# Kernel optimization log

Hardware: AMD Instinct MI355X
Metric: run time of the kernel (lower is better)

Reference implementation:

```python
import jax, jax.numpy as jnp
import numpy as np

N_PER_DEG = 30000
MAX_DEG = 6
MIN_DEG = 0
N_ATOMS = N_PER_DEG * (MAX_DEG + 1)  # 210000, atoms sorted by degree
N_FEAT = 128
NB_FILTER = 128
NB_AFFINE = 2 * MAX_DEG + (1 - MIN_DEG)  # 13


def setup_inputs() -> dict:
    key = jax.random.key(0)
    ks = jax.random.split(key, 2 + MAX_DEG)
    atoms = jax.random.normal(ks[0], (N_ATOMS, N_FEAT), dtype=jnp.float32)
    # glorot-ish scale for the 13 affine weights
    W = jax.random.normal(ks[1], (NB_AFFINE, N_FEAT, NB_FILTER), dtype=jnp.float32) * (1.0 / np.sqrt(N_FEAT))
    b = jnp.zeros((NB_AFFINE, NB_FILTER), dtype=jnp.float32)
    # deg_slice[d] = (start, count) for degree d in 0..MAX_DEG; equal-size buckets
    deg_slice = jnp.asarray(
        np.stack([np.arange(MAX_DEG + 1) * N_PER_DEG,
                  np.full(MAX_DEG + 1, N_PER_DEG)], axis=1).astype(np.int32))
    inp = {"atoms": atoms, "W": W, "b": b, "deg_slice": deg_slice}
    for d in range(1, MAX_DEG + 1):
        inp[f"adj{d}"] = jax.random.randint(ks[1 + d], (N_PER_DEG, d), 0, N_ATOMS, dtype=jnp.int32)
    return inp


def reference(atoms, W, b, deg_slice, adj1, adj2, adj3, adj4, adj5, adj6):
    """Degree-bucketed graph convolution (deepchem GraphConv, linear activation).

    W ordering matches the original iterator: for deg=1..MAX_DEG the pair
    (rel=W[2*(deg-1)], self=W[2*(deg-1)+1]), then deg-0 self uses W[2*MAX_DEG].
    Output concat order: deg 0 bucket first, then deg 1..MAX_DEG.
    """
    adjs = [adj1, adj2, adj3, adj4, adj5, adj6]
    ds = np.asarray(deg_slice)  # structural constant: static slice bounds
    outs = [None] * (MAX_DEG + 1 - MIN_DEG)
    # deg 0: self-affine only
    s0, c0 = int(ds[0, 0]), int(ds[0, 1])
    outs[0] = atoms[s0:s0 + c0] @ W[2 * MAX_DEG] + b[2 * MAX_DEG]
    for deg in range(1, MAX_DEG + 1):
        s, c = int(ds[deg, 0]), int(ds[deg, 1])
        # gather neighbors of each degree-deg atom and sum: (c, deg, F) -> (c, F)
        rel = jnp.take(atoms, adjs[deg - 1], axis=0).sum(axis=1)
        out = (rel @ W[2 * (deg - 1)] + b[2 * (deg - 1)]
               + atoms[s:s + c] @ W[2 * (deg - 1) + 1] + b[2 * (deg - 1) + 1])
        outs[deg] = out
    return jnp.concatenate(outs, axis=0)  # (N_ATOMS, NB_FILTER)
```

## Files before the change

### kernel.cpp

```cpp
#include <hip/hip_runtime.h>
#include <hip/hip_bf16.h>

#define NPD 30000
#define NF  128
#define MAXDEG 6
#define LDK2 264

typedef __attribute__((ext_vector_type(8))) short short8;
typedef __attribute__((ext_vector_type(4))) float floatx4;

__device__ __forceinline__ unsigned short f2bf(float f) {
    __hip_bfloat16 h = __float2bfloat16(f);
    return __builtin_bit_cast(unsigned short, h);
}
__device__ __forceinline__ uint4 pack16B(float4 a, float4 b) {
    uint4 v;
    v.x = (unsigned)f2bf(a.x) | ((unsigned)f2bf(a.y) << 16);
    v.y = (unsigned)f2bf(a.z) | ((unsigned)f2bf(a.w) << 16);
    v.z = (unsigned)f2bf(b.x) | ((unsigned)f2bf(b.y) << 16);
    v.w = (unsigned)f2bf(b.z) | ((unsigned)f2bf(b.w) << 16);
    return v;
}

__global__ __launch_bounds__(256) void wt_kernel(const float* __restrict__ W,
                                                 unsigned short* __restrict__ Wt) {
    __shared__ unsigned short t[32][33];
    const int bx = blockIdx.x;
    const int a  = bx >> 4;
    const int k0 = ((bx >> 2) & 3) * 32, n0 = (bx & 3) * 32;
    const int tx = threadIdx.x & 31, ty = threadIdx.x >> 5;
    const float*    Wp  = W  + (size_t)a * NF * NF;
    unsigned short* Wtp = Wt + (size_t)a * NF * NF;
#pragma unroll
    for (int i = 0; i < 32; i += 8)
        t[ty + i][tx] = f2bf(Wp[(size_t)(k0 + ty + i) * NF + (n0 + tx)]);
    __syncthreads();
#pragma unroll
    for (int i = 0; i < 32; i += 8)
        Wtp[(size_t)(n0 + ty + i) * NF + (k0 + tx)] = t[tx][ty + i];
}

template <int DEG>
__device__ __forceinline__ void fused_work(
    const float* __restrict__ atoms, const unsigned short* __restrict__ Wt,
    const float* __restrict__ bvec, const int* __restrict__ adj,
    float* __restrict__ out, unsigned short* __restrict__ sA)
{
    const int tid  = threadIdx.x;
    const int lane = tid & 63, wave = tid >> 6;
    const int nb = lane & 15;
    const int kq = (lane >> 4) * 8;
    const int col0 = wave * 32;
    const int row0 = blockIdx.x * 32;
    const int valid = min(32, NPD - row0);
    const int row0g = DEG * NPD + row0;
    const int wi_self = (DEG == 0) ? 12 : (2 * DEG - 1);
    const int wi_rel  = (DEG > 0) ? 2 * (DEG - 1) : 0;

    const int r0 = tid >> 4,          ch0 = (tid & 15) * 8;
    const int r1 = (tid >> 4) + 16,   ch1 = ch0;
    const int rr0 = min(r0, valid - 1), rr1 = min(r1, valid - 1);
    const float4* sp0 = (const float4*)(atoms + (size_t)(row0g + rr0) * NF + ch0);
    const float4* sp1 = (const float4*)(atoms + (size_t)(row0g + rr1) * NF + ch1);
    float4 sv0 = sp0[0], sv1 = sp0[1], sv2 = sp1[0], sv3 = sp1[1];

    if constexpr (DEG > 0) {
        const int gr  = tid >> 3;
        const int gc  = (tid & 7) * 16;
        const int grr = min(gr, valid - 1);
        const int* arow = adj + (size_t)(row0 + grr) * DEG;
        int idxs[DEG];
#pragma unroll
        for (int j = 0; j < DEG; ++j) idxs[j] = arow[j];

        *(uint4*)&sA[r0 * LDK2 + ch0] = pack16B(sv0, sv1);
        *(uint4*)&sA[r1 * LDK2 + ch1] = pack16B(sv2, sv3);

        float s[16];
#pragma unroll
        for (int i = 0; i < 16; ++i) s[i] = 0.f;
        float4 q0, q1, q2, q3, n0, n1, n2, n3;
        {
            const float4* p = (const float4*)(atoms + (size_t)idxs[0] * NF + gc);
            q0 = p[0]; q1 = p[1]; q2 = p[2]; q3 = p[3];
        }
#pragma unroll
        for (int j = 0; j < DEG; ++j) {
            if (j + 1 < DEG) {
                const float4* p = (const float4*)(atoms + (size_t)idxs[j + 1] * NF + gc);
                n0 = p[0]; n1 = p[1]; n2 = p[2]; n3 = p[3];
            }
            s[0]  += q0.x; s[1]  += q0.y; s[2]  += q0.z; s[3]  += q0.w;
            s[4]  += q1.x; s[5]  += q1.y; s[6]  += q1.z; s[7]  += q1.w;
            s[8]  += q2.x; s[9]  += q2.y; s[10] += q2.z; s[11] += q2.w;
            s[12] += q3.x; s[13] += q3.y; s[14] += q3.z; s[15] += q3.w;
            q0 = n0; q1 = n1; q2 = n2; q3 = n3;
        }
        uint4 w0 = pack16B(make_float4(s[0], s[1], s[2], s[3]),
                           make_float4(s[4], s[5], s[6], s[7]));
        uint4 w1 = pack16B(make_float4(s[8], s[9], s[10], s[11]),
                           make_float4(s[12], s[13], s[14], s[15]));
        *(uint4*)&sA[gr * LDK2 + NF + gc]     = w0;
        *(uint4*)&sA[gr * LDK2 + NF + gc + 8] = w1;
    } else {
        *(uint4*)&sA[r0 * LDK2 + ch0] = pack16B(sv0, sv1);
        *(uint4*)&sA[r1 * LDK2 + ch1] = pack16B(sv2, sv3);
    }
    __syncthreads();

    floatx4 acc[2][2];
#pragma unroll
    for (int i = 0; i < 2; i++)
#pragma unroll
        for (int j = 0; j < 2; j++) acc[i][j] = (floatx4){0.f, 0.f, 0.f, 0.f};

    constexpr int NKK = (DEG > 0) ? 8 : 4;
#pragma unroll
    for (int kk = 0; kk < NKK; ++kk) {
        const int wi = (kk < 4) ? wi_self : wi_rel;
        const unsigned short* Wp = Wt + (size_t)wi * NF * NF;
        short8 bfr[2];
#pragma unroll
        for (int nt = 0; nt < 2; ++nt)
            bfr[nt] = *(const short8*)(Wp + (size_t)(col0 + nt * 16 + nb) * NF
                                          + (kk & 3) * 32 + kq);
        short8 af[2];
#pragma unroll
        for (int mt = 0; mt < 2; ++mt)
            af[mt] = *(const short8*)&sA[(mt * 16 + nb) * LDK2 + kk * 32 + kq];
#pragma unroll
        for (int mt = 0; mt < 2; ++mt)
#pragma unroll
            for (int nt = 0; nt < 2; ++nt)
                acc[mt][nt] = __builtin_amdgcn_mfma_f32_16x16x32_bf16(
                    af[mt], bfr[nt], acc[mt][nt], 0, 0, 0);
    }

    float bias[2];
#pragma unroll
    for (int nt = 0; nt < 2; ++nt) {
        const int n = col0 + nt * 16 + nb;
        float bv = bvec[wi_self * NF + n];
        if (DEG > 0) bv += bvec[wi_rel * NF + n];
        bias[nt] = bv;
    }
    const int rq = (lane >> 4) * 4;
#pragma unroll
    for (int mt = 0; mt < 2; ++mt) {
#pragma unroll
        for (int reg = 0; reg < 4; ++reg) {
            const int r = mt * 16 + rq + reg;
            if (r < valid) {
                float* op = out + (size_t)(row0g + r) * NF;
#pragma unroll
                for (int nt = 0; nt < 2; ++nt)
                    __builtin_nontemporal_store(acc[mt][nt][reg] + bias[nt],
                                                op + col0 + nt * 16 + nb);
            }
        }
    }
}

__global__ __launch_bounds__(256) void fused_kernel(
    const float* __restrict__ atoms, const unsigned short* __restrict__ Wt,
    const float* __restrict__ bvec,
    const int* __restrict__ adj1, const int* __restrict__ adj2,
    const int* __restrict__ adj3, const int* __restrict__ adj4,
    const int* __restrict__ adj5, const int* __restrict__ adj6,
    float* __restrict__ out)
{
    __shared__ unsigned short sA[32 * LDK2];
    switch (blockIdx.y) {
        case 0: fused_work<0>(atoms, Wt, bvec, nullptr, out, sA); break;
        case 1: fused_work<1>(atoms, Wt, bvec, adj1,    out, sA); break;
        case 2: fused_work<2>(atoms, Wt, bvec, adj2,    out, sA); break;
        case 3: fused_work<3>(atoms, Wt, bvec, adj3,    out, sA); break;
        case 4: fused_work<4>(atoms, Wt, bvec, adj4,    out, sA); break;
        case 5: fused_work<5>(atoms, Wt, bvec, adj5,    out, sA); break;
        default: fused_work<6>(atoms, Wt, bvec, adj6,   out, sA); break;
    }
}

__global__ __launch_bounds__(128) void naive_kernel(
    const float* __restrict__ atoms, const float* __restrict__ W,
    const float* __restrict__ b,
    const int* __restrict__ adj1, const int* __restrict__ adj2,
    const int* __restrict__ adj3, const int* __restrict__ adj4,
    const int* __restrict__ adj5, const int* __restrict__ adj6,
    float* __restrict__ out)
{
    const int i = blockIdx.x;
    const int deg = i / NPD, r = i - deg * NPD, n = threadIdx.x;
    __shared__ float selfr[NF], relr[NF];
    selfr[n] = atoms[(size_t)i * NF + n];
    float rv = 0.f;
    if (deg > 0) {
        const int* adjs[6] = {adj1, adj2, adj3, adj4, adj5, adj6};
        const int* adj = adjs[deg - 1];
        for (int j = 0; j < deg; ++j)
            rv += atoms[(size_t)adj[(size_t)r * deg + j] * NF + n];
    }
    relr[n] = rv;
    __syncthreads();
    const int ws  = (deg == 0) ? 12 : 2 * deg - 1;
    const int wrl = 2 * (deg - 1);
    float acc = b[ws * NF + n] + ((deg > 0) ? b[wrl * NF + n] : 0.f);
    for (int k = 0; k < NF; ++k) {
        acc += selfr[k] * W[(size_t)ws * NF * NF + (size_t)k * NF + n];
        if (deg > 0) acc += relr[k] * W[(size_t)wrl * NF * NF + (size_t)k * NF + n];
    }
    out[(size_t)i * NF + n] = acc;
}

extern "C" void kernel_launch(void* const* d_in, const int* in_sizes, int n_in,
                              void* d_out, int out_size, void* d_ws, size_t ws_size,
                              hipStream_t stream) {
    const float* atoms = (const float*)d_in[0];
    const float* W     = (const float*)d_in[1];
    const float* b     = (const float*)d_in[2];
    const int* adj1 = (const int*)d_in[4];
    const int* adj2 = (const int*)d_in[5];
    const int* adj3 = (const int*)d_in[6];
    const int* adj4 = (const int*)d_in[7];
    const int* adj5 = (const int*)d_in[8];
    const int* adj6 = (const int*)d_in[9];

    const size_t wt_bytes = (size_t)13 * NF * NF * sizeof(unsigned short);

    if (ws_size >= wt_bytes) {
        unsigned short* Wt = (unsigned short*)d_ws;
        wt_kernel<<<208, 256, 0, stream>>>(W, Wt);
        const int gx = (NPD + 31) / 32;
        fused_kernel<<<dim3(gx, 7), 256, 0, stream>>>(
            atoms, Wt, b, adj1, adj2, adj3, adj4, adj5, adj6, (float*)d_out);
    } else {
        naive_kernel<<<NPD * (MAXDEG + 1), NF, 0, stream>>>(
            atoms, W, b, adj1, adj2, adj3, adj4, adj5, adj6, (float*)d_out);
    }
}
```

Baseline: 269.6 us.

## Pre-convert atoms to bf16 in a prep pass and gather bf16 rows

Adds a prep kernel that converts the whole atoms matrix to bf16 in workspace, merged with the weight transpose into one launch. The fused kernel then loads self rows and gathered neighbour rows as bf16, halving gather bytes, and issues all neighbour loads up front before accumulating. The cost is an extra full read of fp32 atoms plus a bf16 write. Neighbour sums now use bf16-rounded inputs, which adds rounding error before accumulation.

```diff
diff --git a/kernel.cpp b/kernel.cpp
--- a/kernel.cpp
+++ b/kernel.cpp
@@ -6,12 +6,18 @@
 #define MAXDEG 6
 #define LDK2 264
 
+#define CVT_BLOCKS 13125
+#define WT_BLOCKS  208
+
 typedef __attribute__((ext_vector_type(8))) short short8;
 typedef __attribute__((ext_vector_type(4))) float floatx4;
 
 __device__ __forceinline__ unsigned short f2bf(float f) {
     __hip_bfloat16 h = __float2bfloat16(f);
     return __builtin_bit_cast(unsigned short, h);
+}
+__device__ __forceinline__ float bf2f(unsigned short u) {
+    unsigned v = ((unsigned)u) << 16; return __builtin_bit_cast(float, v);
 }
 __device__ __forceinline__ uint4 pack16B(float4 a, float4 b) {
     uint4 v;
@@ -21,30 +27,55 @@
     v.w = (unsigned)f2bf(b.z) | ((unsigned)f2bf(b.w) << 16);
     return v;
 }
-
-__global__ __launch_bounds__(256) void wt_kernel(const float* __restrict__ W,
-                                                 unsigned short* __restrict__ Wt) {
+__device__ __forceinline__ uint4 pack16Bv(floatx4 a, floatx4 b) {
+    uint4 v;
+    v.x = (unsigned)f2bf(a.x) | ((unsigned)f2bf(a.y) << 16);
+    v.y = (unsigned)f2bf(a.z) | ((unsigned)f2bf(a.w) << 16);
+    v.z = (unsigned)f2bf(b.x) | ((unsigned)f2bf(b.y) << 16);
+    v.w = (unsigned)f2bf(b.z) | ((unsigned)f2bf(b.w) << 16);
+    return v;
+}
+__device__ __forceinline__ void addu4(float* s, uint4 h) {
+    s[0] += bf2f((unsigned short)h.x); s[1] += bf2f((unsigned short)(h.x >> 16));
+    s[2] += bf2f((unsigned short)h.y); s[3] += bf2f((unsigned short)(h.y >> 16));
+    s[4] += bf2f((unsigned short)h.z); s[5] += bf2f((unsigned short)(h.z >> 16));
+    s[6] += bf2f((unsigned short)h.w); s[7] += bf2f((unsigned short)(h.w >> 16));
+}
+
+__global__ __launch_bounds__(256) void prep_kernel(
+    const float* __restrict__ atoms, const float* __restrict__ W,
+    unsigned short* __restrict__ atomsH, unsigned short* __restrict__ Wt)
+{
     __shared__ unsigned short t[32][33];
     const int bx = blockIdx.x;
-    const int a  = bx >> 4;
-    const int k0 = ((bx >> 2) & 3) * 32, n0 = (bx & 3) * 32;
-    const int tx = threadIdx.x & 31, ty = threadIdx.x >> 5;
-    const float*    Wp  = W  + (size_t)a * NF * NF;
-    unsigned short* Wtp = Wt + (size_t)a * NF * NF;
-#pragma unroll
-    for (int i = 0; i < 32; i += 8)
-        t[ty + i][tx] = f2bf(Wp[(size_t)(k0 + ty + i) * NF + (n0 + tx)]);
-    __syncthreads();
-#pragma unroll
-    for (int i = 0; i < 32; i += 8)
-        Wtp[(size_t)(n0 + ty + i) * NF + (k0 + tx)] = t[tx][ty + i];
-}
-
-template <int DEG>
+    if (bx < WT_BLOCKS) {
+        const int a  = bx >> 4;
+        const int k0 = ((bx >> 2) & 3) * 32, n0 = (bx & 3) * 32;
+        const int tx = threadIdx.x & 31, ty = threadIdx.x >> 5;
+        const float*    Wp  = W  + (size_t)a * NF * NF;
+        unsigned short* Wtp = Wt + (size_t)a * NF * NF;
+#pragma unroll
+        for (int i = 0; i < 32; i += 8)
+            t[ty + i][tx] = f2bf(Wp[(size_t)(k0 + ty + i) * NF + (n0 + tx)]);
+        __syncthreads();
+#pragma unroll
+        for (int i = 0; i < 32; i += 8)
+            Wtp[(size_t)(n0 + ty + i) * NF + (k0 + tx)] = t[tx][ty + i];
+    } else {
+        const size_t i = (size_t)(bx - WT_BLOCKS) * 256 + threadIdx.x;
+        const floatx4* p = (const floatx4*)(atoms + i * 8);
+        floatx4 a = __builtin_nontemporal_load(p);
+        floatx4 b = __builtin_nontemporal_load(p + 1);
+        ((uint4*)atomsH)[i] = pack16Bv(a, b);
+    }
+}
+
+template <int DEG, bool BF16A>
 __device__ __forceinline__ void fused_work(
-    const float* __restrict__ atoms, const unsigned short* __restrict__ Wt,
-    const float* __restrict__ bvec, const int* __restrict__ adj,
-    float* __restrict__ out, unsigned short* __restrict__ sA)
+    const float* __restrict__ atomsF, const unsigned short* __restrict__ atomsH,
+    const unsigned short* __restrict__ Wt, const float* __restrict__ bvec,
+    const int* __restrict__ adj, float* __restrict__ out,
+    unsigned short* __restrict__ sA)
 {
     const int tid  = threadIdx.x;
     const int lane = tid & 63, wave = tid >> 6;
@@ -57,12 +88,21 @@
     const int wi_self = (DEG == 0) ? 12 : (2 * DEG - 1);
     const int wi_rel  = (DEG > 0) ? 2 * (DEG - 1) : 0;
 
-    const int r0 = tid >> 4,          ch0 = (tid & 15) * 8;
-    const int r1 = (tid >> 4) + 16,   ch1 = ch0;
+    const int r0 = tid >> 4,        ch0 = (tid & 15) * 8;
+    const int r1 = r0 + 16;
     const int rr0 = min(r0, valid - 1), rr1 = min(r1, valid - 1);
-    const float4* sp0 = (const float4*)(atoms + (size_t)(row0g + rr0) * NF + ch0);
-    const float4* sp1 = (const float4*)(atoms + (size_t)(row0g + rr1) * NF + ch1);
-    float4 sv0 = sp0[0], sv1 = sp0[1], sv2 = sp1[0], sv3 = sp1[1];
+    if (BF16A) {
+        uint4 s0 = *(const uint4*)(atomsH + (size_t)(row0g + rr0) * NF + ch0);
+        uint4 s1 = *(const uint4*)(atomsH + (size_t)(row0g + rr1) * NF + ch0);
+        *(uint4*)&sA[r0 * LDK2 + ch0] = s0;
+        *(uint4*)&sA[r1 * LDK2 + ch0] = s1;
+    } else {
+        const float4* sp0 = (const float4*)(atomsF + (size_t)(row0g + rr0) * NF + ch0);
+        const float4* sp1 = (const float4*)(atomsF + (size_t)(row0g + rr1) * NF + ch0);
+        float4 a0 = sp0[0], a1 = sp0[1], a2 = sp1[0], a3 = sp1[1];
+        *(uint4*)&sA[r0 * LDK2 + ch0] = pack16B(a0, a1);
+        *(uint4*)&sA[r1 * LDK2 + ch0] = pack16B(a2, a3);
+    }
 
     if constexpr (DEG > 0) {
         const int gr  = tid >> 3;
@@ -73,28 +113,41 @@
 #pragma unroll
         for (int j = 0; j < DEG; ++j) idxs[j] = arow[j];
 
-        *(uint4*)&sA[r0 * LDK2 + ch0] = pack16B(sv0, sv1);
-        *(uint4*)&sA[r1 * LDK2 + ch1] = pack16B(sv2, sv3);
-
         float s[16];
 #pragma unroll
         for (int i = 0; i < 16; ++i) s[i] = 0.f;
-        float4 q0, q1, q2, q3, n0, n1, n2, n3;
-        {
-            const float4* p = (const float4*)(atoms + (size_t)idxs[0] * NF + gc);
-            q0 = p[0]; q1 = p[1]; q2 = p[2]; q3 = p[3];
-        }
-#pragma unroll
-        for (int j = 0; j < DEG; ++j) {
-            if (j + 1 < DEG) {
-                const float4* p = (const float4*)(atoms + (size_t)idxs[j + 1] * NF + gc);
-                n0 = p[0]; n1 = p[1]; n2 = p[2]; n3 = p[3];
-            }
-            s[0]  += q0.x; s[1]  += q0.y; s[2]  += q0.z; s[3]  += q0.w;
-            s[4]  += q1.x; s[5]  += q1.y; s[6]  += q1.z; s[7]  += q1.w;
-            s[8]  += q2.x; s[9]  += q2.y; s[10] += q2.z; s[11] += q2.w;
-            s[12] += q3.x; s[13] += q3.y; s[14] += q3.z; s[15] += q3.w;
-            q0 = n0; q1 = n1; q2 = n2; q3 = n3;
+
+        if (BF16A) {
+            uint4 ga[DEG], gb[DEG];
+#pragma unroll
+            for (int j = 0; j < DEG; ++j) {
+                const unsigned short* base = atomsH + (size_t)idxs[j] * NF + gc;
+                ga[j] = *(const uint4*)base;
+                gb[j] = *(const uint4*)(base + 8);
+            }
+#pragma unroll
+            for (int j = 0; j < DEG; ++j) {
+                addu4(s, ga[j]);
+                addu4(s + 8, gb[j]);
+            }
+        } else {
+            float4 q0, q1, q2, q3, n0, n1, n2, n3;
+            {
+                const float4* p = (const float4*)(atomsF + (size_t)idxs[0] * NF + gc);
+                q0 = p[0]; q1 = p[1]; q2 = p[2]; q3 = p[3];
+            }
+#pragma unroll
+            for (int j = 0; j < DEG; ++j) {
+                if (j + 1 < DEG) {
+                    const float4* p = (const float4*)(atomsF + (size_t)idxs[j + 1] * NF + gc);
+                    n0 = p[0]; n1 = p[1]; n2 = p[2]; n3 = p[3];
+                }
+                s[0]  += q0.x; s[1]  += q0.y; s[2]  += q0.z; s[3]  += q0.w;
+                s[4]  += q1.x; s[5]  += q1.y; s[6]  += q1.z; s[7]  += q1.w;
+                s[8]  += q2.x; s[9]  += q2.y; s[10] += q2.z; s[11] += q2.w;
+                s[12] += q3.x; s[13] += q3.y; s[14] += q3.z; s[15] += q3.w;
+                q0 = n0; q1 = n1; q2 = n2; q3 = n3;
+            }
         }
         uint4 w0 = pack16B(make_float4(s[0], s[1], s[2], s[3]),
                            make_float4(s[4], s[5], s[6], s[7]));
@@ -102,9 +155,6 @@
                            make_float4(s[12], s[13], s[14], s[15]));
         *(uint4*)&sA[gr * LDK2 + NF + gc]     = w0;
         *(uint4*)&sA[gr * LDK2 + NF + gc + 8] = w1;
-    } else {
-        *(uint4*)&sA[r0 * LDK2 + ch0] = pack16B(sv0, sv1);
-        *(uint4*)&sA[r1 * LDK2 + ch1] = pack16B(sv2, sv3);
     }
     __syncthreads();
 
@@ -161,9 +211,10 @@
     }
 }
 
+template <bool BF16A>
 __global__ __launch_bounds__(256) void fused_kernel(
-    const float* __restrict__ atoms, const unsigned short* __restrict__ Wt,
-    const float* __restrict__ bvec,
+    const float* __restrict__ atomsF, const unsigned short* __restrict__ atomsH,
+    const unsigned short* __restrict__ Wt, const float* __restrict__ bvec,
     const int* __restrict__ adj1, const int* __restrict__ adj2,
     const int* __restrict__ adj3, const int* __restrict__ adj4,
     const int* __restrict__ adj5, const int* __restrict__ adj6,
@@ -171,13 +222,13 @@
 {
     __shared__ unsigned short sA[32 * LDK2];
     switch (blockIdx.y) {
-        case 0: fused_work<0>(atoms, Wt, bvec, nullptr, out, sA); break;
-        case 1: fused_work<1>(atoms, Wt, bvec, adj1,    out, sA); break;
-        case 2: fused_work<2>(atoms, Wt, bvec, adj2,    out, sA); break;
-        case 3: fused_work<3>(atoms, Wt, bvec, adj3,    out, sA); break;
-        case 4: fused_work<4>(atoms, Wt, bvec, adj4,    out, sA); break;
-        case 5: fused_work<5>(atoms, Wt, bvec, adj5,    out, sA); break;
-        default: fused_work<6>(atoms, Wt, bvec, adj6,   out, sA); break;
+        case 0: fused_work<0, BF16A>(atomsF, atomsH, Wt, bvec, nullptr, out, sA); break;
+        case 1: fused_work<1, BF16A>(atomsF, atomsH, Wt, bvec, adj1,    out, sA); break;
+        case 2: fused_work<2, BF16A>(atomsF, atomsH, Wt, bvec, adj2,    out, sA); break;
+        case 3: fused_work<3, BF16A>(atomsF, atomsH, Wt, bvec, adj3,    out, sA); break;
+        case 4: fused_work<4, BF16A>(atomsF, atomsH, Wt, bvec, adj4,    out, sA); break;
+        case 5: fused_work<5, BF16A>(atomsF, atomsH, Wt, bvec, adj5,    out, sA); break;
+        default: fused_work<6, BF16A>(atomsF, atomsH, Wt, bvec, adj6,   out, sA); break;
     }
 }
 
@@ -226,13 +277,20 @@
     const int* adj6 = (const int*)d_in[9];
 
     const size_t wt_bytes = (size_t)13 * NF * NF * sizeof(unsigned short);
-
-    if (ws_size >= wt_bytes) {
+    const size_t at_bytes = (size_t)NPD * (MAXDEG + 1) * NF * sizeof(unsigned short);
+    const int gx = (NPD + 31) / 32;
+
+    if (ws_size >= wt_bytes + at_bytes) {
+        unsigned short* Wt     = (unsigned short*)d_ws;
+        unsigned short* atomsH = (unsigned short*)((char*)d_ws + wt_bytes);
+        prep_kernel<<<WT_BLOCKS + CVT_BLOCKS, 256, 0, stream>>>(atoms, W, atomsH, Wt);
+        fused_kernel<true><<<dim3(gx, 7), 256, 0, stream>>>(
+            atoms, atomsH, Wt, b, adj1, adj2, adj3, adj4, adj5, adj6, (float*)d_out);
+    } else if (ws_size >= wt_bytes) {
         unsigned short* Wt = (unsigned short*)d_ws;
-        wt_kernel<<<208, 256, 0, stream>>>(W, Wt);
-        const int gx = (NPD + 31) / 32;
-        fused_kernel<<<dim3(gx, 7), 256, 0, stream>>>(
-            atoms, Wt, b, adj1, adj2, adj3, adj4, adj5, adj6, (float*)d_out);
+        prep_kernel<<<WT_BLOCKS, 256, 0, stream>>>(atoms, W, nullptr, Wt);
+        fused_kernel<false><<<dim3(gx, 7), 256, 0, stream>>>(
+            atoms, nullptr, Wt, b, adj1, adj2, adj3, adj4, adj5, adj6, (float*)d_out);
     } else {
         naive_kernel<<<NPD * (MAXDEG + 1), NF, 0, stream>>>(
             atoms, W, b, adj1, adj2, adj3, adj4, adj5, adj6, (float*)d_out);
```

Measured after the change: 264.7 us. No clear change (-1.8%).
